# Performance work log

Measured on AMD Instinct MI355X. Metric: run time of the kernel, lower is better.

## Reference

```python
import jax, jax.numpy as jnp
import numpy as np

B, C, H, W, K = 2, 3, 256, 256, 51  # output H,W; filter size K; input is (H+K-1, W+K-1)


def _sepconv(inp, vertical, horizontal):
    # inp: [B,C,H+K-1,W+K-1]; vertical/horizontal: [B,K,H,W]
    Kf = vertical.shape[1]
    Ho, Wo = vertical.shape[2], vertical.shape[3]
    rows = jnp.stack([inp[:, :, i:i + Ho, :] for i in range(Kf)], axis=0)

    def body(acc, j):
        # window for horizontal offset j: [K,B,C,Ho,Wo]
        win = jax.lax.dynamic_slice_in_dim(rows, j, Wo, axis=4)
        # contract over vertical taps i with per-pixel vertical kernel
        vcon = jnp.einsum('kbchw,bkhw->bchw', win, vertical)
        # weight by per-pixel horizontal tap j and accumulate
        acc = acc + vcon * horizontal[:, j][:, None, :, :]
        return acc, None

    acc0 = jnp.zeros((inp.shape[0], inp.shape[1], Ho, Wo), inp.dtype)
    out, _ = jax.lax.scan(body, acc0, jnp.arange(Kf))
    return out


def setup_inputs() -> dict:
    key = jax.random.key(0)
    k1, k2, k3 = jax.random.split(key, 3)
    tenInput = jax.random.normal(k1, (B, C, H + K - 1, W + K - 1), dtype=jnp.float32)
    tenVertical = jax.random.normal(k2, (B, K, H, W), dtype=jnp.float32)
    tenHorizontal = jax.random.normal(k3, (B, K, H, W), dtype=jnp.float32)
    return {"tenInput": tenInput, "tenVertical": tenVertical, "tenHorizontal": tenHorizontal}


def reference(tenInput, tenVertical, tenHorizontal):
    return _sepconv(tenInput, tenVertical, tenHorizontal)
```

## Files before the change

### kernel.cpp

```cpp
#include <hip/hip_runtime.h>


namespace {
constexpr int KK = 51;
constexpr int NB = 2;
constexpr int NC = 3;
constexpr int HH = 256;
constexpr int WW = 256;
constexpr int IN_H = HH + KK - 1;
constexpr int IN_W = WW + KK - 1;

constexpr int TILE_W = 32;
constexpr int TILE_H = 8;
constexpr int NTX = 8;
constexpr int R = 4;
constexpr int NTY = 8;
constexpr int NS = 4;
constexpr int NTHREADS = NTX * NTY * NS;
constexpr int HALO_W = TILE_W + KK - 1;
constexpr int LDS_W = 84;
constexpr int LDS_H = TILE_H + KK - 1;
constexpr int KSTRIDE = HH * WW;
}

__device__ __forceinline__ float fget(const float4 v, int i) {
  return (i == 0) ? v.x : (i == 1) ? v.y : (i == 2) ? v.z : v.w;
}

__global__ __launch_bounds__(NTHREADS, 1)
void sepconv_kernel(
    const float* __restrict__ inp,
    const float* __restrict__ vert,
    const float* __restrict__ horiz,
    float* __restrict__ out)
{
  __shared__ float lds[LDS_H * LDS_W];

  const int tid = threadIdx.x;
  const int tx  = tid & (NTX - 1);
  const int ty  = (tid >> 3) & (NTY - 1);
  const int s   = tid >> 6;

  const int x0 = blockIdx.x * TILE_W;
  const int y0 = blockIdx.y * TILE_H;
  const int bc = blockIdx.z;
  const int b  = bc / NC;
  const int c  = bc % NC;

  {
    const float* src = inp + (((size_t)(b * NC + c)) * IN_H + y0) * IN_W + x0;
    constexpr int total2 = LDS_H * (HALO_W / 2);
    for (int e = tid; e < total2; e += NTHREADS) {
      const int col2 = e % (HALO_W / 2);
      const int r    = e / (HALO_W / 2);
      const float2 v = *reinterpret_cast<const float2*>(src + (size_t)r * IN_W + col2 * 2);
      float* dst = &lds[r * LDS_W + col2 * 2];
      dst[0] = v.x; dst[1] = v.y;
    }
    for (int e = tid; e < LDS_H * 2; e += NTHREADS) {
      const int r = e >> 1;
      const int p = e & 1;
      lds[r * LDS_W + HALO_W + p] = 0.0f;
    }
  }
  __syncthreads();

  const int lx = tx * R;
  const int xg = x0 + lx;
  const int yg = y0 + ty;

  float acc[R] = {0.f, 0.f, 0.f, 0.f};

  const int blk0 = (s == 0) ? 0 : (3 * s + 1);
  const int nblk = (s == 0) ? 4 : 3;

  const float* vbase = vert  + (((size_t)b * KK) * HH + yg) * WW + xg;
  const float* hbase = horiz + (((size_t)b * KK) * HH + yg) * WW + xg;

#pragma unroll 1
  for (int t = 0; t < nblk; ++t) {
    const int ibase = (blk0 + t) * 4;

    float4 v4[4];
    float  w[4][8];
#pragma unroll
    for (int ib = 0; ib < 4; ++ib) {
      const int iv = ibase + ib;
      const int ic = (iv <= 50) ? iv : 50;
      float4 vv = *reinterpret_cast<const float4*>(vbase + (size_t)ic * KSTRIDE);
      if (iv > 50) vv = make_float4(0.f, 0.f, 0.f, 0.f);
      v4[ib] = vv;
      const int rr = ty + ic;
      const float4* p = reinterpret_cast<const float4*>(&lds[rr * LDS_W + lx]);
      const float4 a = p[0], bq = p[1];
      w[ib][0] = a.x;  w[ib][1] = a.y;  w[ib][2] = a.z;  w[ib][3] = a.w;
      w[ib][4] = bq.x; w[ib][5] = bq.y; w[ib][6] = bq.z; w[ib][7] = bq.w;
    }

    const float* hp = hbase;

#pragma unroll 1
    for (int j0 = 0; j0 < 48; j0 += 4) {
      float4 h4[4];
#pragma unroll
      for (int jj = 0; jj < 4; ++jj)
        h4[jj] = *reinterpret_cast<const float4*>(hp + (size_t)jj * KSTRIDE);

#pragma unroll
      for (int jj = 0; jj < 4; ++jj) {
#pragma unroll
        for (int rx = 0; rx < R; ++rx) {
          float tv = fget(v4[0], rx) * w[0][rx + jj];
          tv = fmaf(fget(v4[1], rx), w[1][rx + jj], tv);
          tv = fmaf(fget(v4[2], rx), w[2][rx + jj], tv);
          tv = fmaf(fget(v4[3], rx), w[3][rx + jj], tv);
          acc[rx] = fmaf(fget(h4[jj], rx), tv, acc[rx]);
        }
      }

      const int rbase = lx + j0 + 8;
#pragma unroll
      for (int ib = 0; ib < 4; ++ib) {
        const int iv = ibase + ib;
        const int ic = (iv <= 50) ? iv : 50;
        const int rr = ty + ic;
#pragma unroll
        for (int q = 0; q < 4; ++q) w[ib][q] = w[ib][q + 4];
        const float4 n = *reinterpret_cast<const float4*>(&lds[rr * LDS_W + rbase]);
        w[ib][4] = n.x; w[ib][5] = n.y; w[ib][6] = n.z; w[ib][7] = n.w;
      }
      hp += (size_t)4 * KSTRIDE;
    }

    {
      float4 h4e[3];
#pragma unroll
      for (int jj = 0; jj < 3; ++jj)
        h4e[jj] = *reinterpret_cast<const float4*>(hp + (size_t)jj * KSTRIDE);
#pragma unroll
      for (int jj = 0; jj < 3; ++jj) {
#pragma unroll
        for (int rx = 0; rx < R; ++rx) {
          float tv = fget(v4[0], rx) * w[0][rx + jj];
          tv = fmaf(fget(v4[1], rx), w[1][rx + jj], tv);
          tv = fmaf(fget(v4[2], rx), w[2][rx + jj], tv);
          tv = fmaf(fget(v4[3], rx), w[3][rx + jj], tv);
          acc[rx] = fmaf(fget(h4e[jj], rx), tv, acc[rx]);
        }
      }
    }
  }

  __syncthreads();
  if (s > 0) {
    float* p = &lds[((s - 1) * 64 + ty * NTX + tx) * 4];
#pragma unroll
    for (int rx = 0; rx < R; ++rx) p[rx] = acc[rx];
  }
  __syncthreads();
  if (s == 0) {
#pragma unroll
    for (int g = 0; g < 3; ++g) {
      const float* p = &lds[(g * 64 + ty * NTX + tx) * 4];
#pragma unroll
      for (int rx = 0; rx < R; ++rx) acc[rx] += p[rx];
    }
    const float4 o = make_float4(acc[0], acc[1], acc[2], acc[3]);
    *reinterpret_cast<float4*>(out + (((size_t)(b * NC + c)) * HH + yg) * WW + xg) = o;
  }
}

extern "C" void kernel_launch(void* const* d_in, const int* in_sizes, int n_in,
                              void* d_out, int out_size, void* d_ws, size_t ws_size,
                              hipStream_t stream) {
  const float* inp   = (const float*)d_in[0];
  const float* vert  = (const float*)d_in[1];
  const float* horiz = (const float*)d_in[2];
  float* out = (float*)d_out;

  dim3 grid(WW / TILE_W, HH / TILE_H, NB * NC);
  sepconv_kernel<<<grid, NTHREADS, 0, stream>>>(inp, vert, horiz, out);
}
```

Measured before the change: 159.0 us.

## Double per-thread output width to 8 pixels with rotating float4 LDS window

Widens each thread's register tile from 4 to 8 output columns, and the block tile from 32 to 64 columns, so each LDS input load and each vertical-tap product feeds more outputs. The input window is now held as a 3-slot rotating ring of float4 registers, indexed through compile-time templates, which removes the per-step register shifting. The grid is halved, leaving fewer blocks (96 → 48×... fewer) to fill the GPU, and register pressure rises. The zero-padding of the extra LDS columns is dropped.

```diff
diff --git a/kernel.cpp b/kernel.cpp
--- a/kernel.cpp
+++ b/kernel.cpp
@@ -10,21 +10,61 @@
 constexpr int IN_H = HH + KK - 1;
 constexpr int IN_W = WW + KK - 1;
 
-constexpr int TILE_W = 32;
+constexpr int TILE_W = 64;
 constexpr int TILE_H = 8;
 constexpr int NTX = 8;
-constexpr int R = 4;
+constexpr int R = 8;
 constexpr int NTY = 8;
 constexpr int NS = 4;
 constexpr int NTHREADS = NTX * NTY * NS;
 constexpr int HALO_W = TILE_W + KK - 1;
-constexpr int LDS_W = 84;
+constexpr int LDS_W = 116;
 constexpr int LDS_H = TILE_H + KK - 1;
 constexpr int KSTRIDE = HH * WW;
 }
 
 __device__ __forceinline__ float fget(const float4 v, int i) {
   return (i == 0) ? v.x : (i == 1) ? v.y : (i == 2) ? v.z : v.w;
+}
+
+template <int P, int JJ>
+__device__ __forceinline__ void fma_jtap(const float4 (&v4)[4][2], const float4 (&w4)[4][3],
+                                         const float4 ha, const float4 hb, float (&acc)[R]) {
+#pragma unroll
+  for (int rx = 0; rx < R; ++rx) {
+    const int k  = rx + JJ;
+    const int sl = (P + k / 4) % 3;
+    const int cp = k & 3;
+    const int vh = rx >> 2, vc = rx & 3;
+    float tv = fget(v4[0][vh], vc) * fget(w4[0][sl], cp);
+    tv = fmaf(fget(v4[1][vh], vc), fget(w4[1][sl], cp), tv);
+    tv = fmaf(fget(v4[2][vh], vc), fget(w4[2][sl], cp), tv);
+    tv = fmaf(fget(v4[3][vh], vc), fget(w4[3][sl], cp), tv);
+    const float hv = (rx < 4) ? fget(ha, vc) : fget(hb, vc);
+    acc[rx] = fmaf(hv, tv, acc[rx]);
+  }
+}
+
+template <int P>
+__device__ __forceinline__ void do_chunk(const float4 (&v4)[4][2], float4 (&w4)[4][3],
+                                         const int (&woff)[4], int ldcol,
+                                         const float* hp, float (&acc)[R],
+                                         const float* smem) {
+  const float4 h0a = *reinterpret_cast<const float4*>(hp);
+  const float4 h0b = *reinterpret_cast<const float4*>(hp + 4);
+  const float4 h1a = *reinterpret_cast<const float4*>(hp + KSTRIDE);
+  const float4 h1b = *reinterpret_cast<const float4*>(hp + KSTRIDE + 4);
+  fma_jtap<P, 0>(v4, w4, h0a, h0b, acc);
+  const float4 h2a = *reinterpret_cast<const float4*>(hp + 2 * (size_t)KSTRIDE);
+  const float4 h2b = *reinterpret_cast<const float4*>(hp + 2 * (size_t)KSTRIDE + 4);
+  const float4 h3a = *reinterpret_cast<const float4*>(hp + 3 * (size_t)KSTRIDE);
+  const float4 h3b = *reinterpret_cast<const float4*>(hp + 3 * (size_t)KSTRIDE + 4);
+  fma_jtap<P, 1>(v4, w4, h1a, h1b, acc);
+  fma_jtap<P, 2>(v4, w4, h2a, h2b, acc);
+  fma_jtap<P, 3>(v4, w4, h3a, h3b, acc);
+#pragma unroll
+  for (int ib = 0; ib < 4; ++ib)
+    w4[ib][P] = *reinterpret_cast<const float4*>(&smem[woff[ib] + ldcol]);
 }
 
 __global__ __launch_bounds__(NTHREADS, 1)
@@ -57,11 +97,6 @@
       float* dst = &lds[r * LDS_W + col2 * 2];
       dst[0] = v.x; dst[1] = v.y;
     }
-    for (int e = tid; e < LDS_H * 2; e += NTHREADS) {
-      const int r = e >> 1;
-      const int p = e & 1;
-      lds[r * LDS_W + HALO_W + p] = 0.0f;
-    }
   }
   __syncthreads();
 
@@ -69,7 +104,9 @@
   const int xg = x0 + lx;
   const int yg = y0 + ty;
 
-  float acc[R] = {0.f, 0.f, 0.f, 0.f};
+  float acc[R];
+#pragma unroll
+  for (int rx = 0; rx < R; ++rx) acc[rx] = 0.f;
 
   const int blk0 = (s == 0) ? 0 : (3 * s + 1);
   const int nblk = (s == 0) ? 4 : 3;
@@ -81,79 +118,48 @@
   for (int t = 0; t < nblk; ++t) {
     const int ibase = (blk0 + t) * 4;
 
-    float4 v4[4];
-    float  w[4][8];
+    float4 v4[4][2];
+    float4 w4[4][3];
+    int    woff[4];
 #pragma unroll
     for (int ib = 0; ib < 4; ++ib) {
       const int iv = ibase + ib;
       const int ic = (iv <= 50) ? iv : 50;
-      float4 vv = *reinterpret_cast<const float4*>(vbase + (size_t)ic * KSTRIDE);
-      if (iv > 50) vv = make_float4(0.f, 0.f, 0.f, 0.f);
-      v4[ib] = vv;
-      const int rr = ty + ic;
-      const float4* p = reinterpret_cast<const float4*>(&lds[rr * LDS_W + lx]);
-      const float4 a = p[0], bq = p[1];
-      w[ib][0] = a.x;  w[ib][1] = a.y;  w[ib][2] = a.z;  w[ib][3] = a.w;
-      w[ib][4] = bq.x; w[ib][5] = bq.y; w[ib][6] = bq.z; w[ib][7] = bq.w;
+      float4 va = *reinterpret_cast<const float4*>(vbase + (size_t)ic * KSTRIDE);
+      float4 vb = *reinterpret_cast<const float4*>(vbase + (size_t)ic * KSTRIDE + 4);
+      if (iv > 50) { va = make_float4(0.f, 0.f, 0.f, 0.f); vb = va; }
+      v4[ib][0] = va; v4[ib][1] = vb;
+      woff[ib] = (ty + ic) * LDS_W;
+      const float4* p = reinterpret_cast<const float4*>(&lds[woff[ib] + lx]);
+      w4[ib][0] = p[0]; w4[ib][1] = p[1]; w4[ib][2] = p[2];
     }
 
     const float* hp = hbase;
 
 #pragma unroll 1
-    for (int j0 = 0; j0 < 48; j0 += 4) {
-      float4 h4[4];
-#pragma unroll
-      for (int jj = 0; jj < 4; ++jj)
-        h4[jj] = *reinterpret_cast<const float4*>(hp + (size_t)jj * KSTRIDE);
-
-#pragma unroll
-      for (int jj = 0; jj < 4; ++jj) {
-#pragma unroll
-        for (int rx = 0; rx < R; ++rx) {
-          float tv = fget(v4[0], rx) * w[0][rx + jj];
-          tv = fmaf(fget(v4[1], rx), w[1][rx + jj], tv);
-          tv = fmaf(fget(v4[2], rx), w[2][rx + jj], tv);
-          tv = fmaf(fget(v4[3], rx), w[3][rx + jj], tv);
-          acc[rx] = fmaf(fget(h4[jj], rx), tv, acc[rx]);
-        }
-      }
-
-      const int rbase = lx + j0 + 8;
-#pragma unroll
-      for (int ib = 0; ib < 4; ++ib) {
-        const int iv = ibase + ib;
-        const int ic = (iv <= 50) ? iv : 50;
-        const int rr = ty + ic;
-#pragma unroll
-        for (int q = 0; q < 4; ++q) w[ib][q] = w[ib][q + 4];
-        const float4 n = *reinterpret_cast<const float4*>(&lds[rr * LDS_W + rbase]);
-        w[ib][4] = n.x; w[ib][5] = n.y; w[ib][6] = n.z; w[ib][7] = n.w;
-      }
-      hp += (size_t)4 * KSTRIDE;
+    for (int cc = 0; cc < 4; ++cc) {
+      const int base = lx + 12 * cc + 12;
+      do_chunk<0>(v4, w4, woff, base + 0, hp, acc, lds); hp += 4 * (size_t)KSTRIDE;
+      do_chunk<1>(v4, w4, woff, base + 4, hp, acc, lds); hp += 4 * (size_t)KSTRIDE;
+      do_chunk<2>(v4, w4, woff, base + 8, hp, acc, lds); hp += 4 * (size_t)KSTRIDE;
     }
 
     {
-      float4 h4e[3];
-#pragma unroll
-      for (int jj = 0; jj < 3; ++jj)
-        h4e[jj] = *reinterpret_cast<const float4*>(hp + (size_t)jj * KSTRIDE);
-#pragma unroll
-      for (int jj = 0; jj < 3; ++jj) {
-#pragma unroll
-        for (int rx = 0; rx < R; ++rx) {
-          float tv = fget(v4[0], rx) * w[0][rx + jj];
-          tv = fmaf(fget(v4[1], rx), w[1][rx + jj], tv);
-          tv = fmaf(fget(v4[2], rx), w[2][rx + jj], tv);
-          tv = fmaf(fget(v4[3], rx), w[3][rx + jj], tv);
-          acc[rx] = fmaf(fget(h4e[jj], rx), tv, acc[rx]);
-        }
-      }
+      const float4 e0a = *reinterpret_cast<const float4*>(hp);
+      const float4 e0b = *reinterpret_cast<const float4*>(hp + 4);
+      const float4 e1a = *reinterpret_cast<const float4*>(hp + KSTRIDE);
+      const float4 e1b = *reinterpret_cast<const float4*>(hp + KSTRIDE + 4);
+      const float4 e2a = *reinterpret_cast<const float4*>(hp + 2 * (size_t)KSTRIDE);
+      const float4 e2b = *reinterpret_cast<const float4*>(hp + 2 * (size_t)KSTRIDE + 4);
+      fma_jtap<0, 0>(v4, w4, e0a, e0b, acc);
+      fma_jtap<0, 1>(v4, w4, e1a, e1b, acc);
+      fma_jtap<0, 2>(v4, w4, e2a, e2b, acc);
     }
   }
 
   __syncthreads();
   if (s > 0) {
-    float* p = &lds[((s - 1) * 64 + ty * NTX + tx) * 4];
+    float* p = &lds[((s - 1) * 64 + ty * NTX + tx) * R];
 #pragma unroll
     for (int rx = 0; rx < R; ++rx) p[rx] = acc[rx];
   }
@@ -161,12 +167,13 @@
   if (s == 0) {
 #pragma unroll
     for (int g = 0; g < 3; ++g) {
-      const float* p = &lds[(g * 64 + ty * NTX + tx) * 4];
+      const float* p = &lds[(g * 64 + ty * NTX + tx) * R];
 #pragma unroll
       for (int rx = 0; rx < R; ++rx) acc[rx] += p[rx];
     }
-    const float4 o = make_float4(acc[0], acc[1], acc[2], acc[3]);
-    *reinterpret_cast<float4*>(out + (((size_t)(b * NC + c)) * HH + yg) * WW + xg) = o;
+    float* o = out + (((size_t)(b * NC + c)) * HH + yg) * WW + xg;
+    *reinterpret_cast<float4*>(o)     = make_float4(acc[0], acc[1], acc[2], acc[3]);
+    *reinterpret_cast<float4*>(o + 4) = make_float4(acc[4], acc[5], acc[6], acc[7]);
   }
 }
 
```

After: 159.4 us. About the same (+0.3%).
